# Kernel tuning notes

Hardware: AMD Instinct MI355X
Metric: run time of the kernel (lower is better)

## Reference

```python
import jax, jax.numpy as jnp
import numpy as np

B, F0, D = 2048, 40, 32
LAYER0, LAYER1 = 128, 128  # layer_size=(128,128), split_half=True -> field_nums=[40,64]


def setup_inputs() -> dict:
    key = jax.random.key(0)
    k1, k2, k3 = jax.random.split(key, 3)
    x = jax.random.normal(k1, (B, F0, D), dtype=jnp.float32)
    # TF conv1d filters: [1, F_prev*F0, size]; we store them reshaped [F0, F_prev_fields, size]
    # Layer 0: F_prev = F0 = 40 -> W0 flattened index m = i*F0 + j, i over x0 fields, j over hidden fields
    W0 = jax.random.normal(k2, (F0, F0, LAYER0), dtype=jnp.float32) * 0.05
    b0 = jnp.zeros((LAYER0,), dtype=jnp.float32)
    # Layer 1: F_prev = LAYER0 // 2 = 64 (split_half)
    W1 = jax.random.normal(k3, (F0, LAYER0 // 2, LAYER1), dtype=jnp.float32) * 0.05
    b1 = jnp.zeros((LAYER1,), dtype=jnp.float32)
    return {"x": x, "W0": W0, "b0": b0, "W1": W1, "b1": b1}


def reference(x, W0, b0, W1, b1):
    # CIN layer 0: outer product x0 (x) x0 over fields per embedding dim, then 1x1 conv + bias + relu
    # TF flattens dot_result as index i*F_prev + j, matching W0[i, j, s].
    h0 = jax.nn.relu(jnp.einsum('bid,bjd,ijs->bsd', x, x, W0) + b0[None, :, None])  # (B, 128, D)
    half = LAYER0 // 2
    next_hidden, direct0 = h0[:, :half, :], h0[:, half:, :]  # split_half
    # CIN layer 1 (last layer): all feature maps go to direct connect
    direct1 = jax.nn.relu(
        jnp.einsum('bid,bjd,ijs->bsd', x, next_hidden, W1) + b1[None, :, None]
    )  # (B, 128, D)
    result = jnp.concatenate([direct0, direct1], axis=1)  # (B, 192, D)
    return jnp.sum(result, axis=-1)  # (B, 192)
```

## Files before the change

### kernel.cpp

```cpp
#include <hip/hip_runtime.h>
#include <stdint.h>


typedef __attribute__((ext_vector_type(8))) _Float16 half8;
typedef __attribute__((ext_vector_type(2))) _Float16 half2v;
typedef __attribute__((ext_vector_type(4))) float f32x4;

#define T0 30
#define T1P 81
#define PERIOD 3
#define WBUF 12288

__host__ __device__ constexpr int ic0_of(int t) {
    return (t < 2) ? t : (t < 6) ? (t - 2) : (t < 12) ? (t - 6)
         : (t < 20) ? (t - 12) : (t - 20);
}
__host__ __device__ constexpr int jc0_of(int t) {
    return (t < 2) ? 0 : (t < 6) ? 1 : (t < 12) ? 2 : (t < 20) ? 3 : 4;
}

__device__ __forceinline__ unsigned short f2h(float f) {
    return __builtin_bit_cast(unsigned short, (_Float16)f);
}
__device__ __forceinline__ float qsum(float v) {
    v += __shfl_xor(v, 16, 64);
    v += __shfl_xor(v, 32, 64);
    return v;
}
__device__ __forceinline__ void gl_lds16(const unsigned short* g, unsigned short* l) {
    __builtin_amdgcn_global_load_lds(
        (const __attribute__((address_space(1))) unsigned int*)g,
        (__attribute__((address_space(3))) unsigned int*)l,
        16, 0, 0);
}

__global__ void permute_w_both(const float* __restrict__ W0, const float* __restrict__ W1,
                               unsigned short* __restrict__ Wp0, unsigned short* __restrict__ Wp1)
{
    const int t = blockIdx.x;
    const int tid = threadIdx.x;
    unsigned short outv[16];
    unsigned short* dst;
    if (t < T0) {
        const int ic = ic0_of(t), jc = jc0_of(t);
        #pragma unroll
        for (int q = 0; q < 16; ++q) {
            int pos  = tid * 16 + q;
            int oc   = pos & 7, lane = (pos >> 3) & 63;
            int nt   = (pos >> 9) & 3, sh = pos >> 11;
            int s    = sh * 64 + nt * 16 + (lane & 15);
            int i    = ic * 4 + (lane >> 4), j = jc * 8 + oc;
            float v = 0.0f;
            if (i < j)       v = W0[((size_t)(i * 40 + j)) * 128 + s]
                               + W0[((size_t)(j * 40 + i)) * 128 + s];
            else if (i == j) v = W0[((size_t)(i * 40 + i)) * 128 + s];
            outv[q] = f2h(v);
        }
        dst = Wp0 + (size_t)t * 4096 + tid * 16;
    } else {
        const int tt = t - T0;
        if (tt == 80) {
            #pragma unroll
            for (int q = 0; q < 16; ++q) outv[q] = 0;
        } else {
            const int jc = tt / 10, ic = tt % 10;
            #pragma unroll
            for (int q = 0; q < 16; ++q) {
                int pos  = tid * 16 + q;
                int oc   = pos & 7, lane = (pos >> 3) & 63;
                int nt   = (pos >> 9) & 3, sh = pos >> 11;
                int s    = sh * 64 + nt * 16 + (lane & 15);
                int i    = ic * 4 + (lane >> 4), j = jc * 8 + oc;
                outv[q] = f2h(W1[((size_t)(i * 64 + j)) * 128 + s]);
            }
        }
        dst = Wp1 + (size_t)tt * 4096 + tid * 16;
    }
    *(uint4*)dst       = *(const uint4*)outv;
    *(uint4*)(dst + 8) = *(const uint4*)(outv + 8);
}

template<int T, int PHASE>
__device__ __forceinline__ void gemm_phase(
    const unsigned short* __restrict__ Wp,
    const unsigned short* __restrict__ Jl,
    int jstride,
    const unsigned int xi_pk[10],
    unsigned short* Wb,
    f32x4 acc[2][4], int tid)
{
    const int lane = tid & 63;
    const int wv = tid >> 6;
    const int rt = wv & 3;
    const int sh = wv >> 2;
    const int ml = lane & 15;

    const unsigned short* jrow0 = Jl + (rt * 32 + ml) * jstride;
    const unsigned short* jrow1 = jrow0 + 16 * jstride;

    const unsigned short* brd = Wb + sh * 2048 + lane * 8;
    const unsigned short* gsrc = Wp + tid * 8;
    unsigned short* ldst = Wb + wv * 512;

    auto stage_period = [&](int buf, int t0) {
        #pragma unroll
        for (int u = 0; u < PERIOD; ++u)
            gl_lds16(gsrc + (size_t)(t0 + u) * 4096, ldst + buf * WBUF + u * 4096);
    };

    stage_period(0, 0);
    __syncthreads();

    uint4 jv0, jv1;
    constexpr int NP = T / PERIOD;
    #pragma unroll
    for (int p = 0; p < NP; ++p) {
        const int cb = p & 1;
        const int nb = cb ^ 1;
        if ((p + 1) * PERIOD < T) stage_period(nb, (p + 1) * PERIOD);
        #pragma unroll
        for (int u = 0; u < PERIOD; ++u) {
            const int t  = p * PERIOD + u;
            const int ic = (PHASE == 0) ? ic0_of(t) : (t % 10);
            const int jc = (PHASE == 0) ? jc0_of(t) : (t / 10);
            const bool rl = (t == 0) ||
                (jc != ((PHASE == 0) ? jc0_of(t - 1) : ((t - 1) / 10)));
            if (rl) {
                jv0 = *(const uint4*)(jrow0 + jc * 8);
                jv1 = *(const uint4*)(jrow1 + jc * 8);
            }
            half2v xp = __builtin_bit_cast(half2v, xi_pk[ic]);
            half2v x0 = {xp[0], xp[0]};
            half2v x1 = {xp[1], xp[1]};
            uint4 av0, av1;
            av0.x = __builtin_bit_cast(unsigned int, (half2v)(x0 * __builtin_bit_cast(half2v, jv0.x)));
            av0.y = __builtin_bit_cast(unsigned int, (half2v)(x0 * __builtin_bit_cast(half2v, jv0.y)));
            av0.z = __builtin_bit_cast(unsigned int, (half2v)(x0 * __builtin_bit_cast(half2v, jv0.z)));
            av0.w = __builtin_bit_cast(unsigned int, (half2v)(x0 * __builtin_bit_cast(half2v, jv0.w)));
            av1.x = __builtin_bit_cast(unsigned int, (half2v)(x1 * __builtin_bit_cast(half2v, jv1.x)));
            av1.y = __builtin_bit_cast(unsigned int, (half2v)(x1 * __builtin_bit_cast(half2v, jv1.y)));
            av1.z = __builtin_bit_cast(unsigned int, (half2v)(x1 * __builtin_bit_cast(half2v, jv1.z)));
            av1.w = __builtin_bit_cast(unsigned int, (half2v)(x1 * __builtin_bit_cast(half2v, jv1.w)));
            #pragma unroll
            for (int nt = 0; nt < 4; ++nt) {
                uint4 bv = *(const uint4*)(brd + cb * WBUF + u * 4096 + nt * 512);
                acc[0][nt] = __builtin_amdgcn_mfma_f32_16x16x32_f16(
                    __builtin_bit_cast(half8, av0),
                    __builtin_bit_cast(half8, bv), acc[0][nt], 0, 0, 0);
                acc[1][nt] = __builtin_amdgcn_mfma_f32_16x16x32_f16(
                    __builtin_bit_cast(half8, av1),
                    __builtin_bit_cast(half8, bv), acc[1][nt], 0, 0, 0);
            }
        }
        __syncthreads();
    }
}

__global__ __launch_bounds__(512, 4)
void fused_two_layer(const float* __restrict__ x,
                     const unsigned short* __restrict__ W0p,
                     const float* __restrict__ b0,
                     const unsigned short* __restrict__ W1p,
                     const float* __restrict__ b1,
                     float* __restrict__ out)
{
    __shared__ __align__(16) unsigned short Xl[128 * 40];
    __shared__ __align__(16) unsigned short NH[128 * 72];
    __shared__ __align__(16) unsigned short Wb[2 * WBUF];

    const int tid  = threadIdx.x;
    const int lane = tid & 63;
    const int wv   = tid >> 6;
    const int rt   = wv & 3;
    const int sh   = wv >> 2;
    const int ml   = lane & 15;
    const int kc   = lane >> 4;

    const float* xblk = x + (size_t)blockIdx.x * (4 * 40 * 32);
    #pragma unroll
    for (int k = 0; k < 10; ++k) {
        int f = 512 * k + tid;
        int bl = f / 1280, rem = f - bl * 1280;
        int i = rem >> 5, d = rem & 31;
        Xl[(bl * 32 + d) * 40 + i] = f2h(xblk[f]);
    }
    __syncthreads();

    unsigned int xi_pk[10];
    {
        const unsigned short* xr0 = Xl + (rt * 32 + ml) * 40;
        const unsigned short* xr1 = xr0 + 16 * 40;
        #pragma unroll
        for (int ic = 0; ic < 10; ++ic) {
            unsigned int u0 = xr0[ic * 4 + kc];
            unsigned int u1 = xr1[ic * 4 + kc];
            xi_pk[ic] = u0 | (u1 << 16);
        }
    }

    f32x4 acc[2][4];
    const f32x4 zero4 = {0.f, 0.f, 0.f, 0.f};
    #pragma unroll
    for (int mt = 0; mt < 2; ++mt)
        #pragma unroll
        for (int nt = 0; nt < 4; ++nt) acc[mt][nt] = zero4;

    gemm_phase<T0, 0>(W0p, Xl, 40, xi_pk, Wb, acc, tid);

    {
        float bias[4];
        #pragma unroll
        for (int nt = 0; nt < 4; ++nt) bias[nt] = b0[sh * 64 + nt * 16 + ml];
        if (sh == 0) {
            #pragma unroll
            for (int mt = 0; mt < 2; ++mt) {
                int r = rt * 32 + mt * 16 + (kc << 2);
                #pragma unroll
                for (int nt = 0; nt < 4; ++nt) {
                    int s = nt * 16 + ml;
                    #pragma unroll
                    for (int rg = 0; rg < 4; ++rg) {
                        float v = fmaxf(acc[mt][nt][rg] + bias[nt], 0.0f);
                        NH[(r + rg) * 72 + s] = f2h(v);
                    }
                }
            }
            {
                int rp = rt * 32 + (lane >> 1);
                int a  = rp * 72 + 64 + (lane & 1) * 4;
                *(unsigned int*)&NH[a]     = 0u;
                *(unsigned int*)&NH[a + 2] = 0u;
            }
        } else {
            int bb = blockIdx.x * 4 + rt;
            #pragma unroll
            for (int nt = 0; nt < 4; ++nt) {
                float sA = 0.f;
                #pragma unroll
                for (int rg = 0; rg < 4; ++rg)
                    sA += fmaxf(acc[0][nt][rg] + bias[nt], 0.f)
                        + fmaxf(acc[1][nt][rg] + bias[nt], 0.f);
                sA = qsum(sA);
                if (lane < 16)
                    out[(size_t)bb * 192 + nt * 16 + lane] = sA;
            }
        }
    }
    __syncthreads();

    #pragma unroll
    for (int mt = 0; mt < 2; ++mt)
        #pragma unroll
        for (int nt = 0; nt < 4; ++nt) acc[mt][nt] = zero4;

    gemm_phase<T1P, 1>(W1p, NH, 72, xi_pk, Wb, acc, tid);

    {
        float bias[4];
        #pragma unroll
        for (int nt = 0; nt < 4; ++nt) bias[nt] = b1[sh * 64 + nt * 16 + ml];
        int bb = blockIdx.x * 4 + rt;
        #pragma unroll
        for (int nt = 0; nt < 4; ++nt) {
            float sA = 0.f;
            #pragma unroll
            for (int rg = 0; rg < 4; ++rg)
                sA += fmaxf(acc[0][nt][rg] + bias[nt], 0.f)
                    + fmaxf(acc[1][nt][rg] + bias[nt], 0.f);
            sA = qsum(sA);
            if (lane < 16)
                out[(size_t)bb * 192 + 64 + sh * 64 + nt * 16 + lane] = sA;
        }
    }
}

extern "C" void kernel_launch(void* const* d_in, const int* in_sizes, int n_in,
                              void* d_out, int out_size, void* d_ws, size_t ws_size,
                              hipStream_t stream) {
    const float* x  = (const float*)d_in[0];
    const float* W0 = (const float*)d_in[1];
    const float* b0 = (const float*)d_in[2];
    const float* W1 = (const float*)d_in[3];
    const float* b1 = (const float*)d_in[4];
    float* out = (float*)d_out;

    unsigned short* W0p = (unsigned short*)d_ws;
    unsigned short* W1p = (unsigned short*)((char*)d_ws + T0 * 4096 * 2);

    permute_w_both<<<T0 + T1P, 256, 0, stream>>>(W0, W1, W0p, W1p);
    fused_two_layer<<<512, 512, 0, stream>>>(x, W0p, b0, W1p, b1, out);
}
```

Baseline: 117.4 us.

## Retile waves to 64 rows by 32 output columns for more B-fragment reuse

Each of the 8 waves now covers 64 rows (four M tiles) by 32 output channels (two N tiles) instead of 32 rows by 64 channels. Each LDS weight fragment now feeds four MFMAs instead of two, which halves B-operand LDS reads per MFMA but doubles the A-side loads and the packed-multiply work per wave. The epilogues, the NH zero-padding and the output indexing are remapped to the new wave layout. Launch bounds drop from 4 to 2 waves-per-EU minimum, giving more registers at the possible cost of occupancy.

```diff
diff --git a/kernel.cpp b/kernel.cpp
--- a/kernel.cpp
+++ b/kernel.cpp
@@ -85,20 +85,19 @@
     const unsigned short* __restrict__ Wp,
     const unsigned short* __restrict__ Jl,
     int jstride,
-    const unsigned int xi_pk[10],
+    const unsigned int xi_pk[2][10],
     unsigned short* Wb,
-    f32x4 acc[2][4], int tid)
+    f32x4 acc[4][2], int tid)
 {
     const int lane = tid & 63;
     const int wv = tid >> 6;
-    const int rt = wv & 3;
-    const int sh = wv >> 2;
+    const int rt = wv & 1;
+    const int sq = wv >> 1;
     const int ml = lane & 15;
 
-    const unsigned short* jrow0 = Jl + (rt * 32 + ml) * jstride;
-    const unsigned short* jrow1 = jrow0 + 16 * jstride;
-
-    const unsigned short* brd = Wb + sh * 2048 + lane * 8;
+    const unsigned short* jbase = Jl + (rt * 64 + ml) * jstride;
+
+    const unsigned short* brd = Wb + (sq >> 1) * 2048 + (sq & 1) * 1024 + lane * 8;
     const unsigned short* gsrc = Wp + tid * 8;
     unsigned short* ldst = Wb + wv * 512;
 
@@ -111,7 +110,7 @@
     stage_period(0, 0);
     __syncthreads();
 
-    uint4 jv0, jv1;
+    uint4 jv[4];
     constexpr int NP = T / PERIOD;
     #pragma unroll
     for (int p = 0; p < NP; ++p) {
@@ -126,37 +125,40 @@
             const bool rl = (t == 0) ||
                 (jc != ((PHASE == 0) ? jc0_of(t - 1) : ((t - 1) / 10)));
             if (rl) {
-                jv0 = *(const uint4*)(jrow0 + jc * 8);
-                jv1 = *(const uint4*)(jrow1 + jc * 8);
-            }
-            half2v xp = __builtin_bit_cast(half2v, xi_pk[ic]);
-            half2v x0 = {xp[0], xp[0]};
-            half2v x1 = {xp[1], xp[1]};
-            uint4 av0, av1;
-            av0.x = __builtin_bit_cast(unsigned int, (half2v)(x0 * __builtin_bit_cast(half2v, jv0.x)));
-            av0.y = __builtin_bit_cast(unsigned int, (half2v)(x0 * __builtin_bit_cast(half2v, jv0.y)));
-            av0.z = __builtin_bit_cast(unsigned int, (half2v)(x0 * __builtin_bit_cast(half2v, jv0.z)));
-            av0.w = __builtin_bit_cast(unsigned int, (half2v)(x0 * __builtin_bit_cast(half2v, jv0.w)));
-            av1.x = __builtin_bit_cast(unsigned int, (half2v)(x1 * __builtin_bit_cast(half2v, jv1.x)));
-            av1.y = __builtin_bit_cast(unsigned int, (half2v)(x1 * __builtin_bit_cast(half2v, jv1.y)));
-            av1.z = __builtin_bit_cast(unsigned int, (half2v)(x1 * __builtin_bit_cast(half2v, jv1.z)));
-            av1.w = __builtin_bit_cast(unsigned int, (half2v)(x1 * __builtin_bit_cast(half2v, jv1.w)));
-            #pragma unroll
-            for (int nt = 0; nt < 4; ++nt) {
+                #pragma unroll
+                for (int mt = 0; mt < 4; ++mt)
+                    jv[mt] = *(const uint4*)(jbase + mt * 16 * jstride + jc * 8);
+            }
+            uint4 av[4];
+            #pragma unroll
+            for (int pr = 0; pr < 2; ++pr) {
+                half2v xp = __builtin_bit_cast(half2v, xi_pk[pr][ic]);
+                half2v x0 = {xp[0], xp[0]};
+                half2v x1 = {xp[1], xp[1]};
+                av[2*pr].x   = __builtin_bit_cast(unsigned int, (half2v)(x0 * __builtin_bit_cast(half2v, jv[2*pr].x)));
+                av[2*pr].y   = __builtin_bit_cast(unsigned int, (half2v)(x0 * __builtin_bit_cast(half2v, jv[2*pr].y)));
+                av[2*pr].z   = __builtin_bit_cast(unsigned int, (half2v)(x0 * __builtin_bit_cast(half2v, jv[2*pr].z)));
+                av[2*pr].w   = __builtin_bit_cast(unsigned int, (half2v)(x0 * __builtin_bit_cast(half2v, jv[2*pr].w)));
+                av[2*pr+1].x = __builtin_bit_cast(unsigned int, (half2v)(x1 * __builtin_bit_cast(half2v, jv[2*pr+1].x)));
+                av[2*pr+1].y = __builtin_bit_cast(unsigned int, (half2v)(x1 * __builtin_bit_cast(half2v, jv[2*pr+1].y)));
+                av[2*pr+1].z = __builtin_bit_cast(unsigned int, (half2v)(x1 * __builtin_bit_cast(half2v, jv[2*pr+1].z)));
+                av[2*pr+1].w = __builtin_bit_cast(unsigned int, (half2v)(x1 * __builtin_bit_cast(half2v, jv[2*pr+1].w)));
+            }
+            #pragma unroll
+            for (int nt = 0; nt < 2; ++nt) {
                 uint4 bv = *(const uint4*)(brd + cb * WBUF + u * 4096 + nt * 512);
-                acc[0][nt] = __builtin_amdgcn_mfma_f32_16x16x32_f16(
-                    __builtin_bit_cast(half8, av0),
-                    __builtin_bit_cast(half8, bv), acc[0][nt], 0, 0, 0);
-                acc[1][nt] = __builtin_amdgcn_mfma_f32_16x16x32_f16(
-                    __builtin_bit_cast(half8, av1),
-                    __builtin_bit_cast(half8, bv), acc[1][nt], 0, 0, 0);
+                #pragma unroll
+                for (int mt = 0; mt < 4; ++mt)
+                    acc[mt][nt] = __builtin_amdgcn_mfma_f32_16x16x32_f16(
+                        __builtin_bit_cast(half8, av[mt]),
+                        __builtin_bit_cast(half8, bv), acc[mt][nt], 0, 0, 0);
             }
         }
         __syncthreads();
     }
 }
 
-__global__ __launch_bounds__(512, 4)
+__global__ __launch_bounds__(512, 2)
 void fused_two_layer(const float* __restrict__ x,
                      const unsigned short* __restrict__ W0p,
                      const float* __restrict__ b0,
@@ -171,8 +173,8 @@
     const int tid  = threadIdx.x;
     const int lane = tid & 63;
     const int wv   = tid >> 6;
-    const int rt   = wv & 3;
-    const int sh   = wv >> 2;
+    const int rt   = wv & 1;
+    const int sq   = wv >> 1;
     const int ml   = lane & 15;
     const int kc   = lane >> 4;
 
@@ -186,38 +188,39 @@
     }
     __syncthreads();
 
-    unsigned int xi_pk[10];
-    {
-        const unsigned short* xr0 = Xl + (rt * 32 + ml) * 40;
+    unsigned int xi_pk[2][10];
+    #pragma unroll
+    for (int pr = 0; pr < 2; ++pr) {
+        const unsigned short* xr0 = Xl + (rt * 64 + pr * 32 + ml) * 40;
         const unsigned short* xr1 = xr0 + 16 * 40;
         #pragma unroll
         for (int ic = 0; ic < 10; ++ic) {
             unsigned int u0 = xr0[ic * 4 + kc];
             unsigned int u1 = xr1[ic * 4 + kc];
-            xi_pk[ic] = u0 | (u1 << 16);
-        }
-    }
-
-    f32x4 acc[2][4];
+            xi_pk[pr][ic] = u0 | (u1 << 16);
+        }
+    }
+
+    f32x4 acc[4][2];
     const f32x4 zero4 = {0.f, 0.f, 0.f, 0.f};
     #pragma unroll
-    for (int mt = 0; mt < 2; ++mt)
-        #pragma unroll
-        for (int nt = 0; nt < 4; ++nt) acc[mt][nt] = zero4;
+    for (int mt = 0; mt < 4; ++mt)
+        #pragma unroll
+        for (int nt = 0; nt < 2; ++nt) acc[mt][nt] = zero4;
 
     gemm_phase<T0, 0>(W0p, Xl, 40, xi_pk, Wb, acc, tid);
 
     {
-        float bias[4];
-        #pragma unroll
-        for (int nt = 0; nt < 4; ++nt) bias[nt] = b0[sh * 64 + nt * 16 + ml];
-        if (sh == 0) {
-            #pragma unroll
-            for (int mt = 0; mt < 2; ++mt) {
-                int r = rt * 32 + mt * 16 + (kc << 2);
+        float bias[2];
+        #pragma unroll
+        for (int nt = 0; nt < 2; ++nt) bias[nt] = b0[sq * 32 + nt * 16 + ml];
+        if (sq < 2) {
+            #pragma unroll
+            for (int mt = 0; mt < 4; ++mt) {
+                int r = rt * 64 + mt * 16 + (kc << 2);
                 #pragma unroll
-                for (int nt = 0; nt < 4; ++nt) {
-                    int s = nt * 16 + ml;
+                for (int nt = 0; nt < 2; ++nt) {
+                    int s = sq * 32 + nt * 16 + ml;
                     #pragma unroll
                     for (int rg = 0; rg < 4; ++rg) {
                         float v = fmaxf(acc[mt][nt][rg] + bias[nt], 0.0f);
@@ -225,51 +228,62 @@
                     }
                 }
             }
-            {
-                int rp = rt * 32 + (lane >> 1);
-                int a  = rp * 72 + 64 + (lane & 1) * 4;
-                *(unsigned int*)&NH[a]     = 0u;
-                *(unsigned int*)&NH[a + 2] = 0u;
-            }
         } else {
-            int bb = blockIdx.x * 4 + rt;
-            #pragma unroll
-            for (int nt = 0; nt < 4; ++nt) {
-                float sA = 0.f;
+            int bb = blockIdx.x * 4 + rt * 2;
+            #pragma unroll
+            for (int nt = 0; nt < 2; ++nt) {
+                float sA = 0.f, sB = 0.f;
                 #pragma unroll
-                for (int rg = 0; rg < 4; ++rg)
+                for (int rg = 0; rg < 4; ++rg) {
                     sA += fmaxf(acc[0][nt][rg] + bias[nt], 0.f)
                         + fmaxf(acc[1][nt][rg] + bias[nt], 0.f);
-                sA = qsum(sA);
-                if (lane < 16)
-                    out[(size_t)bb * 192 + nt * 16 + lane] = sA;
+                    sB += fmaxf(acc[2][nt][rg] + bias[nt], 0.f)
+                        + fmaxf(acc[3][nt][rg] + bias[nt], 0.f);
+                }
+                sA = qsum(sA); sB = qsum(sB);
+                if (lane < 16) {
+                    int col = (sq - 2) * 32 + nt * 16 + lane;
+                    out[(size_t)bb * 192 + col]       = sA;
+                    out[(size_t)(bb + 1) * 192 + col] = sB;
+                }
+            }
+            if (sq == 2) {
+                int a = (rt * 64 + lane) * 72 + 64;
+                *(uint2*)&NH[a]     = (uint2){0u, 0u};
+                *(uint2*)&NH[a + 4] = (uint2){0u, 0u};
             }
         }
     }
     __syncthreads();
 
     #pragma unroll
-    for (int mt = 0; mt < 2; ++mt)
-        #pragma unroll
-        for (int nt = 0; nt < 4; ++nt) acc[mt][nt] = zero4;
+    for (int mt = 0; mt < 4; ++mt)
+        #pragma unroll
+        for (int nt = 0; nt < 2; ++nt) acc[mt][nt] = zero4;
 
     gemm_phase<T1P, 1>(W1p, NH, 72, xi_pk, Wb, acc, tid);
 
     {
-        float bias[4];
-        #pragma unroll
-        for (int nt = 0; nt < 4; ++nt) bias[nt] = b1[sh * 64 + nt * 16 + ml];
-        int bb = blockIdx.x * 4 + rt;
-        #pragma unroll
-        for (int nt = 0; nt < 4; ++nt) {
-            float sA = 0.f;
-            #pragma unroll
-            for (int rg = 0; rg < 4; ++rg)
+        float bias[2];
+        #pragma unroll
+        for (int nt = 0; nt < 2; ++nt) bias[nt] = b1[sq * 32 + nt * 16 + ml];
+        int bb = blockIdx.x * 4 + rt * 2;
+        #pragma unroll
+        for (int nt = 0; nt < 2; ++nt) {
+            float sA = 0.f, sB = 0.f;
+            #pragma unroll
+            for (int rg = 0; rg < 4; ++rg) {
                 sA += fmaxf(acc[0][nt][rg] + bias[nt], 0.f)
                     + fmaxf(acc[1][nt][rg] + bias[nt], 0.f);
-            sA = qsum(sA);
-            if (lane < 16)
-                out[(size_t)bb * 192 + 64 + sh * 64 + nt * 16 + lane] = sA;
+                sB += fmaxf(acc[2][nt][rg] + bias[nt], 0.f)
+                    + fmaxf(acc[3][nt][rg] + bias[nt], 0.f);
+            }
+            sA = qsum(sA); sB = qsum(sB);
+            if (lane < 16) {
+                int col = 64 + sq * 32 + nt * 16 + lane;
+                out[(size_t)bb * 192 + col]       = sA;
+                out[(size_t)(bb + 1) * 192 + col] = sB;
+            }
         }
     }
 }
```

Result: slower. 125.3 us (+6.7%).
